# Performance work log

Measured on AMD Instinct MI355X. Metric: run time of the kernel, lower is better.

The kernel has to match this reference:

```python
import math
import jax, jax.numpy as jnp
import numpy as np

GROUPS = 32
EPS = 1e-5


def group_norm(x, gamma, beta):
    # x: (b, c, h, w); normalize per-group over (c/g, h, w)
    b, c, h, w = x.shape
    xg = x.reshape(b, GROUPS, c // GROUPS, h, w)
    mu = xg.mean(axis=(2, 3, 4), keepdims=True)
    var = xg.var(axis=(2, 3, 4), keepdims=True)
    xn = ((xg - mu) * jax.lax.rsqrt(var + EPS)).reshape(b, c, h, w)
    return xn * gamma[None, :, None, None] + beta[None, :, None, None]


def conv1x1(x, w, bias):
    # x: (b, c, h, w), w: (o, c) -> (b, o, h, w)
    return jnp.einsum('bchw,oc->bohw', x, w) + bias[None, :, None, None]


def setup_inputs() -> dict:
    key = jax.random.key(0)
    ks = jax.random.split(key, 7)
    b, c, h, w = 8, 512, 32, 32
    s = 1.0 / math.sqrt(c)
    return {
        'x': jax.random.normal(ks[0], (b, c, h, w), dtype=jnp.float32),
        'gn_w': jnp.ones((c,), dtype=jnp.float32),
        'gn_b': jnp.zeros((c,), dtype=jnp.float32),
        'qkv_w': jax.random.normal(ks[1], (3 * c, c), dtype=jnp.float32) * s,
        'qkv_b': jnp.zeros((3 * c,), dtype=jnp.float32),
        'proj_w': jax.random.normal(ks[2], (c, c), dtype=jnp.float32) * s,
        'proj_b': jnp.zeros((c,), dtype=jnp.float32),
        'num_heads': 8,
    }


def reference(x, gn_w, gn_b, qkv_w, qkv_b, proj_w, proj_b, num_heads):
    b, c, h, w = x.shape
    hds = num_heads
    d = c // hds
    x_ = group_norm(x, gn_w, gn_b)
    qkv = conv1x1(x_, qkv_w, qkv_b)  # (b, 3c, h, w)
    q, k, v = jnp.split(qkv, 3, axis=1)
    # (b, hds, d, hw)
    q = q.reshape(b, hds, d, h * w)
    k = k.reshape(b, hds, d, h * w)
    v = v.reshape(b, hds, d, h * w)
    # scores: (b, hds, hw, hw) = q^T k / sqrt(d)
    scores = jnp.einsum('bhdq,bhdk->bhqk', q, k) / math.sqrt(d)
    attn = jax.nn.softmax(scores, axis=-1)
    # out = (attn @ v^T)^T -> (b, hds, d, hw)
    out = jnp.einsum('bhqk,bhdk->bhdq', attn, v)
    out = out.reshape(b, c, h, w)
    return x + conv1x1(out, proj_w, proj_b)
```

## Files before the change

### kernel.cpp

```cpp
#include <hip/hip_runtime.h>
#include <hip/hip_bf16.h>


typedef __attribute__((ext_vector_type(8))) short short8v;
typedef __attribute__((ext_vector_type(4))) short short4v;
typedef __attribute__((ext_vector_type(4))) float f32x4;
typedef __attribute__((ext_vector_type(2))) unsigned uint2v;
typedef __attribute__((ext_vector_type(4))) unsigned uint4v;

constexpr int Bn = 8, Cn = 512, HWn = 1024;

#if __has_builtin(__builtin_amdgcn_exp2f)
#define EXP2F(x) __builtin_amdgcn_exp2f(x)
#else
#define EXP2F(x) __exp2f(x)
#endif

static __device__ __forceinline__ unsigned short bf16u(float f) {
  __hip_bfloat16 h = __float2bfloat16(f);
  return __builtin_bit_cast(unsigned short, h);
}
static __device__ __forceinline__ short bf16_of(float f) {
  return (short)bf16u(f);
}
static __device__ __forceinline__ unsigned bf16pk(float a, float b) {
  return (unsigned)bf16u(a) | ((unsigned)bf16u(b) << 16);
}

static __device__ __forceinline__ void gload16(const void* g, void* l) {
  __builtin_amdgcn_global_load_lds(
      (const __attribute__((address_space(1))) unsigned*)g,
      (__attribute__((address_space(3))) unsigned*)l, 16, 0, 0);
}

__global__ __launch_bounds__(256) void gn_fused_k(const float* __restrict__ x,
                                                  const float* __restrict__ gw,
                                                  const float* __restrict__ gb,
                                                  const float* __restrict__ wq,
                                                  const float* __restrict__ wp,
                                                  short* __restrict__ oq,
                                                  short* __restrict__ op,
                                                  short* __restrict__ xn3) {
  const int t = threadIdx.x;
  if (blockIdx.x >= 256) {
    int i = (blockIdx.x - 256) * 256 + t;
    const float* src = wq;
    short* dst = oq;
    int idx = i;
    if (i >= 196608) { src = wp; dst = op; idx = i - 196608; }
    f32x4 v = ((const f32x4*)src)[idx];
    short4v o;
    o.x = bf16_of(v.x); o.y = bf16_of(v.y); o.z = bf16_of(v.z); o.w = bf16_of(v.w);
    *(short4v*)&dst[idx * 4] = o;
    return;
  }
  const int bg = blockIdx.x;
  const int g = bg & 31;
  const f32x4* src = (const f32x4*)(x + (size_t)bg * 16384);
  f32x4 v[16];
  float s = 0.f, ss = 0.f;
#pragma unroll
  for (int k = 0; k < 16; k++) {
    v[k] = src[t + 256 * k];
    s += v[k].x + v[k].y + v[k].z + v[k].w;
    ss += v[k].x * v[k].x + v[k].y * v[k].y + v[k].z * v[k].z + v[k].w * v[k].w;
  }
#pragma unroll
  for (int off = 32; off; off >>= 1) {
    s += __shfl_xor(s, off);
    ss += __shfl_xor(ss, off);
  }
  __shared__ float rs[4], rss[4];
  const int lane = t & 63, w = t >> 6;
  if (lane == 0) { rs[w] = s; rss[w] = ss; }
  __syncthreads();
  const float S = rs[0] + rs[1] + rs[2] + rs[3];
  const float SS = rss[0] + rss[1] + rss[2] + rss[3];
  constexpr float invn = 1.0f / 16384.f;
  const float mu = S * invn;
  const float var = SS * invn - mu * mu;
  const float rstd = rsqrtf(var + 1e-5f);
  float ga[16], be[16];
#pragma unroll
  for (int k = 0; k < 16; k++) {
    ga[k] = gw[g * 16 + k] * rstd;
    be[k] = gb[g * 16 + k] - mu * ga[k];
  }
  short* dst = xn3 + (size_t)bg * 16384;
#pragma unroll
  for (int d = 0; d < 4; d++) {
    unsigned pk[8];
#pragma unroll
    for (int k = 0; k < 16; k += 2)
      pk[k >> 1] = bf16pk(fmaf(v[k][d], ga[k], be[k]),
                          fmaf(v[k + 1][d], ga[k + 1], be[k + 1]));
    uint4v lo = {pk[0], pk[1], pk[2], pk[3]};
    uint4v hi = {pk[4], pk[5], pk[6], pk[7]};
    *(uint4v*)&dst[(4 * t + d) * 16] = lo;
    *(uint4v*)&dst[(4 * t + d) * 16 + 8] = hi;
  }
}

__device__ __forceinline__ short8v frag64(const short* buf, int row, int gk) {
  return *(const short8v*)&buf[row * 64 + ((gk ^ (row & 7)) << 3)];
}
__device__ __forceinline__ short8v frag128(const short* buf, int row, int gk) {
  return *(const short8v*)&buf[row * 128 + ((gk ^ (row & 7)) << 3)];
}

__global__ __launch_bounds__(256, 2) void gemm_qkv_k(
    const short* __restrict__ A, const short* __restrict__ xn3,
    const float* __restrict__ bias, short* __restrict__ oQ,
    short* __restrict__ oK, short* __restrict__ oV) {
  const int bid = blockIdx.x;
  const int swz = (bid & 7) * 96 + (bid >> 3);
  const int bn = swz & 7;
  const int rest = swz >> 3;
  const int bm = rest % 12, b = rest / 12;
  const bool VBLK = (bm >= 8);

  const short* Bb = xn3 + (size_t)b * 524288;
  __shared__ __align__(16) short As[2][8192];
  __shared__ __align__(16) short Bs[2][8192];
  const int t = threadIdx.x, l = t & 63, w = t >> 6;
  const int wr = w >> 1, wc = w & 1;
  const int m0 = bm * 128, n0 = bn * 128;
  const f32x4 vzero = {0.f, 0.f, 0.f, 0.f};
  f32x4 acc[4][4];
#pragma unroll
  for (int i = 0; i < 4; i++)
#pragma unroll
    for (int j = 0; j < 4; j++) acc[i][j] = vzero;

  const int sr0 = t >> 3;
  const int sg = t & 7;

#define STAGE_QKV(buf, k0)                                                    \
  do {                                                                        \
    _Pragma("unroll") for (int it = 0; it < 4; it++) {                        \
      int r = it * 32 + sr0;                                                  \
      int gs = sg ^ (r & 7);                                                  \
      gload16(&A[(size_t)(m0 + r) * 512 + (k0) + gs * 8],                     \
              &As[buf][it * 2048 + w * 512]);                                 \
      int gp = ((k0) >> 4) + (gs >> 1);                                       \
      gload16(&Bb[(size_t)((gp << 10) + n0 + r) * 16 + ((gs & 1) << 3)],      \
              &Bs[buf][it * 2048 + w * 512]);                                 \
    }                                                                         \
  } while (0)

  STAGE_QKV(0, 0);
  __syncthreads();

  for (int ks = 0; ks < 8; ks++) {
    const int cb = ks & 1;
    if (ks < 7) STAGE_QKV(cb ^ 1, (ks + 1) * 64);
#pragma unroll
    for (int kk = 0; kk < 2; kk++) {
      short8v af[4], bf[4];
#pragma unroll
      for (int i = 0; i < 4; i++)
        af[i] = frag64(&As[cb][0], wr * 64 + i * 16 + (l & 15), kk * 4 + (l >> 4));
#pragma unroll
      for (int j = 0; j < 4; j++)
        bf[j] = frag64(&Bs[cb][0], wc * 64 + j * 16 + (l & 15), kk * 4 + (l >> 4));
      if (VBLK) {
#pragma unroll
        for (int i = 0; i < 4; i++)
#pragma unroll
          for (int j = 0; j < 4; j++)
            acc[i][j] = __builtin_amdgcn_mfma_f32_16x16x32_bf16(bf[j], af[i], acc[i][j], 0, 0, 0);
      } else {
#pragma unroll
        for (int i = 0; i < 4; i++)
#pragma unroll
          for (int j = 0; j < 4; j++)
            acc[i][j] = __builtin_amdgcn_mfma_f32_16x16x32_bf16(af[i], bf[j], acc[i][j], 0, 0, 0);
      }
    }
    __syncthreads();
  }

  if (!VBLK) {
    short* oBase = (m0 < 512) ? oQ : oK;
    const int mc = (m0 < 512 ? m0 : m0 - 512) + wr * 64;
#pragma unroll
    for (int i = 0; i < 4; i++) {
      int mi = mc + i * 16 + (l >> 4) * 4;
      f32x4 bv = *(const f32x4*)&bias[m0 + wr * 64 + i * 16 + (l >> 4) * 4];
#pragma unroll
      for (int j = 0; j < 4; j++) {
        int n = n0 + wc * 64 + j * 16 + (l & 15);
        uint2v pk = {bf16pk(acc[i][j][0] + bv[0], acc[i][j][1] + bv[1]),
                     bf16pk(acc[i][j][2] + bv[2], acc[i][j][3] + bv[3])};
        *(uint2v*)&oBase[((size_t)b * HWn + n) * 512 + mi] = pk;
      }
    }
  } else {
#pragma unroll
    for (int i = 0; i < 4; i++) {
      int m = m0 + wr * 64 + i * 16 + (l & 15);
      float bv = bias[m];
      short* vrow = oV + ((size_t)b * 512 + (m - 1024)) * HWn;
#pragma unroll
      for (int j = 0; j < 4; j++) {
        int n = n0 + wc * 64 + j * 16 + (l >> 4) * 4;
        uint2v pk = {bf16pk(acc[i][j][0] + bv, acc[i][j][1] + bv),
                     bf16pk(acc[i][j][2] + bv, acc[i][j][3] + bv)};
        *(uint2v*)&vrow[n] = pk;
      }
    }
  }
}

__global__ __launch_bounds__(512, 2) void gemm_proj_k(
    const short* __restrict__ A, const short* __restrict__ Bt,
    const float* __restrict__ bias, const float* __restrict__ resid,
    float* __restrict__ outF) {
  const int bid = blockIdx.x;
  const int swz = (bid & 7) * 32 + (bid >> 3);
  const int bn = swz & 7;
  const int rest = swz >> 3;
  const int bm = rest & 3, b = rest >> 2;

  const short* Bb = Bt + (size_t)b * HWn * Cn;
  __shared__ __align__(16) short As[2][8192];
  __shared__ __align__(16) short Bs[2][8192];
  const int t = threadIdx.x, l = t & 63, w = t >> 6;
  const int wr = w >> 1, wc = w & 1;
  const int m0 = bm * 128, n0 = bn * 128;
  const f32x4 vzero = {0.f, 0.f, 0.f, 0.f};
  f32x4 acc[2][4];
#pragma unroll
  for (int i = 0; i < 2; i++)
#pragma unroll
    for (int j = 0; j < 4; j++) acc[i][j] = vzero;

  const int sr0 = t >> 3;
  const int sg = t & 7;

#define STAGE_PROJ(buf, k0)                                                   \
  do {                                                                        \
    _Pragma("unroll") for (int it = 0; it < 2; it++) {                        \
      int r = it * 64 + sr0;                                                  \
      int gs = sg ^ (r & 7);                                                  \
      gload16(&A[(size_t)(m0 + r) * 512 + (k0) + gs * 8],                     \
              &As[buf][it * 4096 + w * 512]);                                 \
      gload16(&Bb[(size_t)(n0 + r) * 512 + (k0) + gs * 8],                    \
              &Bs[buf][it * 4096 + w * 512]);                                 \
    }                                                                         \
  } while (0)

  STAGE_PROJ(0, 0);
  __syncthreads();

  for (int ks = 0; ks < 8; ks++) {
    const int cb = ks & 1;
    if (ks < 7) STAGE_PROJ(cb ^ 1, (ks + 1) * 64);
#pragma unroll
    for (int kk = 0; kk < 2; kk++) {
      short8v af[2], bf[4];
#pragma unroll
      for (int i = 0; i < 2; i++)
        af[i] = frag64(&As[cb][0], wr * 32 + i * 16 + (l & 15), kk * 4 + (l >> 4));
#pragma unroll
      for (int j = 0; j < 4; j++)
        bf[j] = frag64(&Bs[cb][0], wc * 64 + j * 16 + (l & 15), kk * 4 + (l >> 4));
#pragma unroll
      for (int i = 0; i < 2; i++)
#pragma unroll
        for (int j = 0; j < 4; j++)
          acc[i][j] = __builtin_amdgcn_mfma_f32_16x16x32_bf16(af[i], bf[j], acc[i][j], 0, 0, 0);
    }
    __syncthreads();
  }

  float* outb = outF + (size_t)b * Cn * HWn;
  const float* rb = resid + (size_t)b * Cn * HWn;
#pragma unroll
  for (int i = 0; i < 2; i++) {
    f32x4 bv = *(const f32x4*)&bias[m0 + wr * 32 + i * 16 + (l >> 4) * 4];
#pragma unroll
    for (int r = 0; r < 4; r++) {
      int m = m0 + wr * 32 + i * 16 + (l >> 4) * 4 + r;
#pragma unroll
      for (int j = 0; j < 4; j++) {
        int n = n0 + wc * 64 + j * 16 + (l & 15);
        size_t idx = (size_t)m * HWn + n;
        outb[idx] = acc[i][j][r] + bv[r] + rb[idx];
      }
    }
  }
}

__global__ __launch_bounds__(256, 2) void attn_k(const short* __restrict__ qT,
                                                 const short* __restrict__ kT,
                                                 const short* __restrict__ vB,
                                                 short* __restrict__ aoT) {
  const int bid = blockIdx.x;
  const int swz = (bid & 7) * 64 + (bid >> 3);
  const int qt = swz & 7, head = (swz >> 3) & 7, b = swz >> 6;
  __shared__ __align__(16) short SM[33792];
  short* Ks = SM;
  short* Vs = SM + 8192;
  short* Ps = SM + 16384;
  const int t = threadIdx.x, l = t & 63, w = t >> 6;
  short* PsA = Ps + (2 * w) * 2176;
  short* PsB = Ps + (2 * w + 1) * 2176;
  const int g = l >> 4;
  const f32x4 vzero = {0.f, 0.f, 0.f, 0.f};

  const short* ksrc = kT + (size_t)b * HWn * 512 + head * 64;
  const short* vsrc = vB + ((size_t)b * 512 + head * 64) * HWn;

  const short* qbase = qT +
      ((size_t)b * HWn + qt * 128 + 32 * w + (l & 15)) * 512 + head * 64 + g * 8;
  const short8v qA0 = *(const short8v*)&qbase[0];
  const short8v qA1 = *(const short8v*)&qbase[32];
  const short8v qB0 = *(const short8v*)&qbase[16 * 512];
  const short8v qB1 = *(const short8v*)&qbase[16 * 512 + 32];

  const int kkv0 = w * 8 + (l >> 3), kg = l & 7;
  const int vd0 = w * 4 + (l >> 4), vg = l & 15;

#pragma unroll
  for (int it = 0; it < 4; it++) {
    int kv = kkv0 + it * 32;
    gload16(&ksrc[(size_t)kv * 512 + (kg ^ (kv & 7)) * 8], &Ks[it * 2048 + w * 512]);
    int d = vd0 + it * 16;
    gload16(&vsrc[(size_t)d * HWn + (vg ^ (d & 7)) * 8], &Vs[it * 2048 + w * 512]);
  }
  __syncthreads();

  f32x4 oaA[4], oaB[4];
#pragma unroll
  for (int f = 0; f < 4; f++) { oaA[f] = vzero; oaB[f] = vzero; }
  float lA = 0.f, lB = 0.f;
  constexpr float SC = 0.1803368801111f;
  constexpr float MOFF = -11.5415602855f;

#pragma unroll 1
  for (int kt = 0; kt < 8; kt++) {
    short8v kreg[4], vreg[4];
    if (kt < 7) {
      const int kt1 = kt + 1;
#pragma unroll
      for (int it = 0; it < 4; it++) {
        int kv = kkv0 + it * 32;
        kreg[it] = *(const short8v*)&ksrc[(size_t)(kt1 * 128 + kv) * 512 +
                                          (kg ^ (kv & 7)) * 8];
        int d = vd0 + it * 16;
        vreg[it] = *(const short8v*)&vsrc[(size_t)d * HWn + kt1 * 128 +
                                          (vg ^ (d & 7)) * 8];
      }
    }

    f32x4 saA[8], saB[8];
    __builtin_amdgcn_s_setprio(1);
#pragma unroll
    for (int f = 0; f < 8; f++) {
      short8v ka0 = frag64(Ks, 16 * f + (l & 15), g);
      short8v ka1 = frag64(Ks, 16 * f + (l & 15), g + 4);
      saA[f] = __builtin_amdgcn_mfma_f32_16x16x32_bf16(ka0, qA0, vzero, 0, 0, 0);
      saB[f] = __builtin_amdgcn_mfma_f32_16x16x32_bf16(ka0, qB0, vzero, 0, 0, 0);
      saA[f] = __builtin_amdgcn_mfma_f32_16x16x32_bf16(ka1, qA1, saA[f], 0, 0, 0);
      saB[f] = __builtin_amdgcn_mfma_f32_16x16x32_bf16(ka1, qB1, saB[f], 0, 0, 0);
    }
    __builtin_amdgcn_s_setprio(0);

    f32x4 psAv = vzero, psBv = vzero;
#pragma unroll
    for (int f = 0; f < 8; f++)
#pragma unroll
      for (int r = 0; r < 4; r++) {
        float eA = EXP2F(fmaf(saA[f][r], SC, MOFF));
        float eB = EXP2F(fmaf(saB[f][r], SC, MOFF));
        saA[f][r] = eA;
        saB[f][r] = eB;
        psAv[r] += eA;
        psBv[r] += eB;
      }
    float psA = (psAv[0] + psAv[1]) + (psAv[2] + psAv[3]);
    float psB = (psBv[0] + psBv[1]) + (psBv[2] + psBv[3]);
    psA += __shfl_xor(psA, 16);
    psA += __shfl_xor(psA, 32);
    psB += __shfl_xor(psB, 16);
    psB += __shfl_xor(psB, 32);
    lA += psA;
    lB += psB;

#pragma unroll
    for (int f = 0; f < 8; f++) {
      int o = (l & 15) * 136 + 16 * f + 4 * g;
      uint2v pkA = {bf16pk(saA[f][0], saA[f][1]), bf16pk(saA[f][2], saA[f][3])};
      uint2v pkB = {bf16pk(saB[f][0], saB[f][1]), bf16pk(saB[f][2], saB[f][3])};
      *(uint2v*)&PsA[o] = pkA;
      *(uint2v*)&PsB[o] = pkB;
    }
    short8v paA[4], paB[4];
#pragma unroll
    for (int c = 0; c < 4; c++) {
      paA[c] = *(const short8v*)&PsA[(l & 15) * 136 + c * 32 + g * 8];
      paB[c] = *(const short8v*)&PsB[(l & 15) * 136 + c * 32 + g * 8];
    }
    __builtin_amdgcn_s_setprio(1);
#pragma unroll
    for (int fd = 0; fd < 4; fd++) {
      int row = 16 * fd + (l & 15);
#pragma unroll
      for (int c = 0; c < 4; c++) {
        short8v vb = frag128(Vs, row, c * 4 + g);
        oaA[fd] = __builtin_amdgcn_mfma_f32_16x16x32_bf16(paA[c], vb, oaA[fd], 0, 0, 0);
        oaB[fd] = __builtin_amdgcn_mfma_f32_16x16x32_bf16(paB[c], vb, oaB[fd], 0, 0, 0);
      }
    }
    __builtin_amdgcn_s_setprio(0);

    if (kt < 7) {
      __syncthreads();
#pragma unroll
      for (int it = 0; it < 4; it++) {
        *(short8v*)&Ks[it * 2048 + w * 512 + l * 8] = kreg[it];
        *(short8v*)&Vs[it * 2048 + w * 512 + l * 8] = vreg[it];
      }
      __syncthreads();
    }
  }

  const float invA = 1.0f / lA, invB = 1.0f / lB;
  float ivA[4], ivB[4];
#pragma unroll
  for (int r = 0; r < 4; r++) {
    ivA[r] = __shfl(invA, 4 * g + r);
    ivB[r] = __shfl(invB, 4 * g + r);
  }
#pragma unroll
  for (int r = 0; r < 4; r++)
#pragma unroll
    for (int f = 0; f < 4; f++) {
      PsA[(4 * g + r) * 136 + 16 * f + (l & 15)] = bf16_of(oaA[f][r] * ivA[r]);
      PsB[(4 * g + r) * 136 + 16 * f + (l & 15)] = bf16_of(oaB[f][r] * ivB[r]);
    }
  __syncthreads();
  short* dst = aoT + ((size_t)b * HWn + qt * 128) * 512 + head * 64;
#pragma unroll
  for (int it = 0; it < 4; it++) {
    int r = (t >> 3) + 32 * it;
    int c8 = (t & 7) * 8;
    *(short8v*)&dst[(size_t)r * 512 + c8] =
        *(const short8v*)&Ps[(r >> 4) * 2176 + (r & 15) * 136 + c8];
  }
}

extern "C" void kernel_launch(void* const* d_in, const int* in_sizes, int n_in,
                              void* d_out, int out_size, void* d_ws, size_t ws_size,
                              hipStream_t stream) {
  const float* x = (const float*)d_in[0];
  const float* gn_w = (const float*)d_in[1];
  const float* gn_b = (const float*)d_in[2];
  const float* qkv_w = (const float*)d_in[3];
  const float* qkv_b = (const float*)d_in[4];
  const float* proj_w = (const float*)d_in[5];
  const float* proj_b = (const float*)d_in[6];
  float* out = (float*)d_out;

  char* ws = (char*)d_ws;
  short* wqb = (short*)(ws + 4096);
  short* wpb = (short*)(ws + 4096 + 1572864);
  char* p = ws + 4096 + 1572864 + 524288;
  const size_t SB = (size_t)Bn * HWn * 512 * 2;
  short* xn3 = (short*)p;
  short* qT = (short*)(p + SB);
  short* kT = (short*)(p + 2 * SB);
  short* vB = (short*)(p + 3 * SB);
  short* aoT = (short*)(p + 4 * SB);

  gn_fused_k<<<1280, 256, 0, stream>>>(x, gn_w, gn_b, qkv_w, proj_w, wqb, wpb, xn3);
  gemm_qkv_k<<<768, 256, 0, stream>>>(wqb, xn3, qkv_b, qT, kT, vB);
  attn_k<<<512, 256, 0, stream>>>(qT, kT, vB, aoT);
  gemm_proj_k<<<256, 512, 0, stream>>>(wpb, aoT, proj_b, x, out);
}
```

Before: 79.94 us.

## Shrink attention KV tile to 64 and raise occupancy to three blocks per CU

The attention kernel now processes keys and values in 64-wide tiles over 16 iterations instead of 128-wide tiles over 8. This cuts shared memory per block from about 66KB to about 34KB, and launch bounds are raised to allow three blocks per CU. The register-staged prefetch of the next tile is replaced by direct global-to-LDS loads between two barriers each iteration, which drops the overlap of loads with compute and doubles the number of syncs. The intent is to hide latency through more resident waves rather than software pipelining.

```diff
diff --git a/kernel.cpp b/kernel.cpp
--- a/kernel.cpp
+++ b/kernel.cpp
@@ -104,9 +104,6 @@
 __device__ __forceinline__ short8v frag64(const short* buf, int row, int gk) {
   return *(const short8v*)&buf[row * 64 + ((gk ^ (row & 7)) << 3)];
 }
-__device__ __forceinline__ short8v frag128(const short* buf, int row, int gk) {
-  return *(const short8v*)&buf[row * 128 + ((gk ^ (row & 7)) << 3)];
-}
 
 __global__ __launch_bounds__(256, 2) void gemm_qkv_k(
     const short* __restrict__ A, const short* __restrict__ xn3,
@@ -292,20 +289,20 @@
   }
 }
 
-__global__ __launch_bounds__(256, 2) void attn_k(const short* __restrict__ qT,
+__global__ __launch_bounds__(256, 3) void attn_k(const short* __restrict__ qT,
                                                  const short* __restrict__ kT,
                                                  const short* __restrict__ vB,
                                                  short* __restrict__ aoT) {
   const int bid = blockIdx.x;
   const int swz = (bid & 7) * 64 + (bid >> 3);
   const int qt = swz & 7, head = (swz >> 3) & 7, b = swz >> 6;
-  __shared__ __align__(16) short SM[33792];
+  __shared__ __align__(16) short SM[17408];
   short* Ks = SM;
-  short* Vs = SM + 8192;
-  short* Ps = SM + 16384;
+  short* Vs = SM + 4096;
+  short* Ps = SM + 8192;
   const int t = threadIdx.x, l = t & 63, w = t >> 6;
-  short* PsA = Ps + (2 * w) * 2176;
-  short* PsB = Ps + (2 * w + 1) * 2176;
+  short* PsA = Ps + (2 * w) * 1152;
+  short* PsB = Ps + (2 * w + 1) * 1152;
   const int g = l >> 4;
   const f32x4 vzero = {0.f, 0.f, 0.f, 0.f};
 
@@ -319,17 +316,7 @@
   const short8v qB0 = *(const short8v*)&qbase[16 * 512];
   const short8v qB1 = *(const short8v*)&qbase[16 * 512 + 32];
 
-  const int kkv0 = w * 8 + (l >> 3), kg = l & 7;
-  const int vd0 = w * 4 + (l >> 4), vg = l & 15;
-
-#pragma unroll
-  for (int it = 0; it < 4; it++) {
-    int kv = kkv0 + it * 32;
-    gload16(&ksrc[(size_t)kv * 512 + (kg ^ (kv & 7)) * 8], &Ks[it * 2048 + w * 512]);
-    int d = vd0 + it * 16;
-    gload16(&vsrc[(size_t)d * HWn + (vg ^ (d & 7)) * 8], &Vs[it * 2048 + w * 512]);
-  }
-  __syncthreads();
+  const int sr = t >> 3, sg = t & 7;
 
   f32x4 oaA[4], oaB[4];
 #pragma unroll
@@ -339,25 +326,23 @@
   constexpr float MOFF = -11.5415602855f;
 
 #pragma unroll 1
-  for (int kt = 0; kt < 8; kt++) {
-    short8v kreg[4], vreg[4];
-    if (kt < 7) {
-      const int kt1 = kt + 1;
-#pragma unroll
-      for (int it = 0; it < 4; it++) {
-        int kv = kkv0 + it * 32;
-        kreg[it] = *(const short8v*)&ksrc[(size_t)(kt1 * 128 + kv) * 512 +
-                                          (kg ^ (kv & 7)) * 8];
-        int d = vd0 + it * 16;
-        vreg[it] = *(const short8v*)&vsrc[(size_t)d * HWn + kt1 * 128 +
-                                          (vg ^ (d & 7)) * 8];
-      }
-    }
-
-    f32x4 saA[8], saB[8];
+  for (int kt = 0; kt < 16; kt++) {
+    __syncthreads();
+#pragma unroll
+    for (int it = 0; it < 2; it++) {
+      int kv = it * 32 + sr;
+      gload16(&ksrc[(size_t)(kt * 64 + kv) * 512 + (sg ^ (kv & 7)) * 8],
+              &Ks[it * 2048 + w * 512]);
+      int d = it * 32 + sr;
+      gload16(&vsrc[(size_t)d * HWn + kt * 64 + (sg ^ (d & 7)) * 8],
+              &Vs[it * 2048 + w * 512]);
+    }
+    __syncthreads();
+
+    f32x4 saA[4], saB[4];
     __builtin_amdgcn_s_setprio(1);
 #pragma unroll
-    for (int f = 0; f < 8; f++) {
+    for (int f = 0; f < 4; f++) {
       short8v ka0 = frag64(Ks, 16 * f + (l & 15), g);
       short8v ka1 = frag64(Ks, 16 * f + (l & 15), g + 4);
       saA[f] = __builtin_amdgcn_mfma_f32_16x16x32_bf16(ka0, qA0, vzero, 0, 0, 0);
@@ -369,7 +354,7 @@
 
     f32x4 psAv = vzero, psBv = vzero;
 #pragma unroll
-    for (int f = 0; f < 8; f++)
+    for (int f = 0; f < 4; f++)
 #pragma unroll
       for (int r = 0; r < 4; r++) {
         float eA = EXP2F(fmaf(saA[f][r], SC, MOFF));
@@ -389,41 +374,31 @@
     lB += psB;
 
 #pragma unroll
-    for (int f = 0; f < 8; f++) {
-      int o = (l & 15) * 136 + 16 * f + 4 * g;
+    for (int f = 0; f < 4; f++) {
+      int o = (l & 15) * 72 + 16 * f + 4 * g;
       uint2v pkA = {bf16pk(saA[f][0], saA[f][1]), bf16pk(saA[f][2], saA[f][3])};
       uint2v pkB = {bf16pk(saB[f][0], saB[f][1]), bf16pk(saB[f][2], saB[f][3])};
       *(uint2v*)&PsA[o] = pkA;
       *(uint2v*)&PsB[o] = pkB;
     }
-    short8v paA[4], paB[4];
-#pragma unroll
-    for (int c = 0; c < 4; c++) {
-      paA[c] = *(const short8v*)&PsA[(l & 15) * 136 + c * 32 + g * 8];
-      paB[c] = *(const short8v*)&PsB[(l & 15) * 136 + c * 32 + g * 8];
+    short8v paA[2], paB[2];
+#pragma unroll
+    for (int c = 0; c < 2; c++) {
+      paA[c] = *(const short8v*)&PsA[(l & 15) * 72 + c * 32 + g * 8];
+      paB[c] = *(const short8v*)&PsB[(l & 15) * 72 + c * 32 + g * 8];
     }
     __builtin_amdgcn_s_setprio(1);
 #pragma unroll
     for (int fd = 0; fd < 4; fd++) {
       int row = 16 * fd + (l & 15);
 #pragma unroll
-      for (int c = 0; c < 4; c++) {
-        short8v vb = frag128(Vs, row, c * 4 + g);
+      for (int c = 0; c < 2; c++) {
+        short8v vb = frag64(Vs, row, c * 4 + g);
         oaA[fd] = __builtin_amdgcn_mfma_f32_16x16x32_bf16(paA[c], vb, oaA[fd], 0, 0, 0);
         oaB[fd] = __builtin_amdgcn_mfma_f32_16x16x32_bf16(paB[c], vb, oaB[fd], 0, 0, 0);
       }
     }
     __builtin_amdgcn_s_setprio(0);
-
-    if (kt < 7) {
-      __syncthreads();
-#pragma unroll
-      for (int it = 0; it < 4; it++) {
-        *(short8v*)&Ks[it * 2048 + w * 512 + l * 8] = kreg[it];
-        *(short8v*)&Vs[it * 2048 + w * 512 + l * 8] = vreg[it];
-      }
-      __syncthreads();
-    }
   }
 
   const float invA = 1.0f / lA, invB = 1.0f / lB;
@@ -433,12 +408,13 @@
     ivA[r] = __shfl(invA, 4 * g + r);
     ivB[r] = __shfl(invB, 4 * g + r);
   }
+  __syncthreads();
 #pragma unroll
   for (int r = 0; r < 4; r++)
 #pragma unroll
     for (int f = 0; f < 4; f++) {
-      PsA[(4 * g + r) * 136 + 16 * f + (l & 15)] = bf16_of(oaA[f][r] * ivA[r]);
-      PsB[(4 * g + r) * 136 + 16 * f + (l & 15)] = bf16_of(oaB[f][r] * ivB[r]);
+      PsA[(4 * g + r) * 72 + 16 * f + (l & 15)] = bf16_of(oaA[f][r] * ivA[r]);
+      PsB[(4 * g + r) * 72 + 16 * f + (l & 15)] = bf16_of(oaB[f][r] * ivB[r]);
     }
   __syncthreads();
   short* dst = aoT + ((size_t)b * HWn + qt * 128) * 512 + head * 64;
@@ -447,7 +423,7 @@
     int r = (t >> 3) + 32 * it;
     int c8 = (t & 7) * 8;
     *(short8v*)&dst[(size_t)r * 512 + c8] =
-        *(const short8v*)&Ps[(r >> 4) * 2176 + (r & 15) * 136 + c8];
+        *(const short8v*)&Ps[(r >> 4) * 1152 + (r & 15) * 72 + c8];
   }
 }
 
```

Measured after the change: 80.25 us. About the same (+0.4%).
